# Performance work log

Measured on AMD Instinct MI355X. Metric: run time of the kernel, lower is better.

The kernel has to match this reference:

```python
import jax, jax.numpy as jnp
import numpy as np
import math

SCALES = [1, 2, 4, 8]
H = 1024           # hidden_size
NS = len(SCALES)
DS = H // NS       # per-scale dim = 256
NH_S = max(1, 8 // NS)  # heads per scale = 2


def _avg_pool(x, s):
    # x: [B, L, d], kernel=stride=s (L divisible by s)
    B, L, d = x.shape
    return x.reshape(B, L // s, s, d).mean(axis=2)


def _mha(q, k, v, in_w, in_b, out_w, out_b, nh):
    # torch nn.MultiheadAttention, batch_first, no mask.
    d = q.shape[-1]
    wq, wk, wv = in_w[:d], in_w[d:2 * d], in_w[2 * d:]
    bq, bk, bv = in_b[:d], in_b[d:2 * d], in_b[2 * d:]
    qh = q @ wq.T + bq
    kh = k @ wk.T + bk
    vh = v @ wv.T + bv
    B, Lq, _ = qh.shape
    Lk = kh.shape[1]
    hd = d // nh
    qh = qh.reshape(B, Lq, nh, hd).transpose(0, 2, 1, 3)
    kh = kh.reshape(B, Lk, nh, hd).transpose(0, 2, 1, 3)
    vh = vh.reshape(B, Lk, nh, hd).transpose(0, 2, 1, 3)
    scores = jnp.einsum('bhqd,bhkd->bhqk', qh, kh) * (1.0 / math.sqrt(hd))
    w = jax.nn.softmax(scores, axis=-1)
    out = jnp.einsum('bhqk,bhkd->bhqd', w, vh)
    out = out.transpose(0, 2, 1, 3).reshape(B, Lq, d)
    out = out @ out_w.T + out_b
    return out, w.mean(axis=1)  # averaged attn weights (torch default)


def setup_inputs() -> dict:
    key = jax.random.key(0)
    ks = jax.random.split(key, 20)
    B, S = 4, 2048
    f = lambda k, shape: (jax.random.normal(k, shape, dtype=jnp.float32) * 0.02)
    return {
        'query': jax.random.normal(ks[0], (B, S, H), dtype=jnp.float32),
        'key': jax.random.normal(ks[1], (B, S, H), dtype=jnp.float32),
        'value': jax.random.normal(ks[2], (B, S, H), dtype=jnp.float32),
        'wq': f(ks[3], (H, H)), 'bq': f(ks[4], (H,)),
        'wk': f(ks[5], (H, H)), 'bk': f(ks[6], (H,)),
        'wv': f(ks[7], (H, H)), 'bv': f(ks[8], (H,)),
        'mha_in_w': f(ks[9], (NS, 3 * DS, DS)),
        'mha_in_b': f(ks[10], (NS, 3 * DS)),
        'mha_out_w': f(ks[11], (NS, DS, DS)),
        'mha_out_b': f(ks[12], (NS, DS)),
        'fus_w': f(ks[13], (H, H)), 'fus_b': f(ks[14], (H,)),
    }


def reference(query, key, value, wq, bq, wk, bk, wv, bv,
              mha_in_w, mha_in_b, mha_out_w, mha_out_b, fus_w, fus_b):
    q = query @ wq.T + bq
    k = key @ wk.T + bk
    v = value @ wv.T + bv
    outs = []
    weights0 = None
    for i, s in enumerate(SCALES):
        qs = q[..., i * DS:(i + 1) * DS]
        ks_ = k[..., i * DS:(i + 1) * DS]
        vs = v[..., i * DS:(i + 1) * DS]
        if s > 1:
            ks_ = _avg_pool(ks_, s)
            vs = _avg_pool(vs, s)
        attended, w = _mha(qs, ks_, vs, mha_in_w[i], mha_in_b[i],
                           mha_out_w[i], mha_out_b[i], NH_S)
        # F.interpolate back to seq_len is an identity here (query length == seq_len)
        outs.append(attended)
        if i == 0:
            weights0 = w
    fused = jnp.concatenate(outs, axis=-1) @ fus_w.T + fus_b
    return fused, weights0
```

## Files before the change

### kernel.cpp

```cpp
#include <hip/hip_runtime.h>
#include <stdint.h>

typedef unsigned short u16;
typedef __bf16 v8bf __attribute__((ext_vector_type(8)));
typedef float v4f __attribute__((ext_vector_type(4)));
typedef __attribute__((address_space(3))) unsigned lds_t;
typedef const __attribute__((address_space(1))) unsigned g_t;

__device__ __forceinline__ u16 f2bf(float f) {
  union { float f; unsigned u; } v; v.f = f;
  unsigned r = v.u + 0x7FFFu + ((v.u >> 16) & 1u);
  return (u16)(r >> 16);
}
__device__ __forceinline__ float bf2f(u16 h) {
  union { unsigned u; float f; } v; v.u = ((unsigned)h) << 16;
  return v.f;
}
__device__ __forceinline__ ushort4 f4bf(float4 f) {
  ushort4 o;
  o.x = f2bf(f.x); o.y = f2bf(f.y); o.z = f2bf(f.z); o.w = f2bf(f.w);
  return o;
}

__global__ void k_cvt(const float* __restrict__ s, u16* __restrict__ d, long n) {
  long i = ((long)blockIdx.x * blockDim.x + threadIdx.x) * 4;
  long stride = (long)gridDim.x * blockDim.x * 4;
  for (; i < n; i += stride) {
    *(ushort4*)(d + i) = f4bf(*(const float4*)(s + i));
  }
}

__global__ void k_cvtpool(const float* __restrict__ src, u16* __restrict__ dst) {
  int g = blockIdx.x & 255, b = blockIdx.x >> 8;
  int c = threadIdx.x * 4;
  const float* p = src + ((long)b * 2048 + g * 8) * 1024 + c;
  u16* df = dst + ((long)b * 2048 + g * 8) * 1024 + c;
  float4 x[8];
#pragma unroll
  for (int j = 0; j < 8; j++) {
    x[j] = *(const float4*)(p + (long)j * 1024);
    *(ushort4*)(df + (long)j * 1024) = f4bf(x[j]);
  }
  float4 s2[4], s4[2], s8;
#pragma unroll
  for (int j = 0; j < 4; j++) {
    s2[j].x = x[2 * j].x + x[2 * j + 1].x;
    s2[j].y = x[2 * j].y + x[2 * j + 1].y;
    s2[j].z = x[2 * j].z + x[2 * j + 1].z;
    s2[j].w = x[2 * j].w + x[2 * j + 1].w;
  }
#pragma unroll
  for (int j = 0; j < 2; j++) {
    s4[j].x = s2[2 * j].x + s2[2 * j + 1].x;
    s4[j].y = s2[2 * j].y + s2[2 * j + 1].y;
    s4[j].z = s2[2 * j].z + s2[2 * j + 1].z;
    s4[j].w = s2[2 * j].w + s2[2 * j + 1].w;
  }
  s8.x = s4[0].x + s4[1].x; s8.y = s4[0].y + s4[1].y;
  s8.z = s4[0].z + s4[1].z; s8.w = s4[0].w + s4[1].w;
  u16* d2 = dst + ((long)8192 + b * 1024 + g * 4) * 1024 + c;
#pragma unroll
  for (int j = 0; j < 4; j++) {
    float4 t = {s2[j].x * 0.5f, s2[j].y * 0.5f, s2[j].z * 0.5f, s2[j].w * 0.5f};
    *(ushort4*)(d2 + (long)j * 1024) = f4bf(t);
  }
  u16* d4 = dst + ((long)12288 + b * 512 + g * 2) * 1024 + c;
#pragma unroll
  for (int j = 0; j < 2; j++) {
    float4 t = {s4[j].x * 0.25f, s4[j].y * 0.25f, s4[j].z * 0.25f, s4[j].w * 0.25f};
    *(ushort4*)(d4 + (long)j * 1024) = f4bf(t);
  }
  float4 t8 = {s8.x * 0.125f, s8.y * 0.125f, s8.z * 0.125f, s8.w * 0.125f};
  *(ushort4*)(dst + ((long)14336 + b * 256 + g) * 1024 + c) = f4bf(t8);
}

__global__ void k_tc(const float* __restrict__ src, u16* __restrict__ dst, int R, int C) {
  __shared__ float t[32][33];
  long zoff = (long)blockIdx.z * R * C;
  int r0 = blockIdx.y * 32, c0 = blockIdx.x * 32;
  int tx = threadIdx.x & 31, ty = threadIdx.x >> 5;
#pragma unroll
  for (int j = 0; j < 32; j += 8)
    t[ty + j][tx] = src[zoff + (long)(r0 + ty + j) * C + c0 + tx];
  __syncthreads();
#pragma unroll
  for (int j = 0; j < 32; j += 8)
    dst[zoff + (long)(c0 + ty + j) * R + r0 + tx] = f2bf(t[tx][ty + j]);
}

__global__ void k_bcomb_qkv(const float* __restrict__ in_w, const float* __restrict__ in_b,
                            const float* __restrict__ bq, const float* __restrict__ bk,
                            const float* __restrict__ bv, float* __restrict__ out) {
  int gw = (blockIdx.x * 256 + threadIdx.x) >> 6;
  int lane = threadIdx.x & 63;
  int p = gw >> 10, j = gw & 1023, i = j >> 8, of = j & 255;
  const float* bp = p == 0 ? bq : p == 1 ? bk : bv;
  const float* row = in_w + ((long)i * 768 + p * 256 + of) * 256;
  float s = 0.f;
#pragma unroll
  for (int m = 0; m < 4; m++) s += row[lane + m * 64] * bp[i * 256 + lane + m * 64];
#pragma unroll
  for (int m = 32; m >= 1; m >>= 1) s += __shfl_xor(s, m, 64);
  if (lane == 0) out[gw] = in_b[(long)i * 768 + p * 256 + of] + s;
}

__global__ void k_bcomb_f(const float* __restrict__ fw, const float* __restrict__ fb,
                          const float* __restrict__ ob, float* __restrict__ out) {
  int w = (blockIdx.x * 256 + threadIdx.x) >> 6;
  int lane = threadIdx.x & 63;
  const float* row = fw + (long)w * 1024;
  float s = 0.f;
  for (int k = lane; k < 1024; k += 64) s += row[k] * ob[k];
#pragma unroll
  for (int m = 32; m >= 1; m >>= 1) s += __shfl_xor(s, m, 64);
  if (lane == 0) out[w] = fb[w] + s;
}

__global__ __launch_bounds__(256) void k_ml0(
    const u16* __restrict__ QHf, const u16* __restrict__ KH,
    float* __restrict__ M0, float* __restrict__ L0)
{
  int z = blockIdx.z;
  int b = z >> 1, h = z & 1;
  int q0 = blockIdx.y * 64;
  __shared__ u16 KV[2][128][32];
  __shared__ float red[2][4][64];

  const int tid = threadIdx.x, lane = tid & 63, wave = tid >> 6;
  const int q4 = lane >> 4, l16 = lane & 15;
  const int wr = (wave >> 1) * 32, wc = (wave & 1) * 64;
  const int srow = wave * 16 + (lane >> 2), scol = (lane & 3) * 8;
  const float alpha = 0.08838834764831845f;

  v8bf qf[2][4];
#pragma unroll
  for (int mi = 0; mi < 2; mi++)
#pragma unroll
    for (int sub = 0; sub < 4; sub++)
      qf[mi][sub] = *(const v8bf*)(QHf + ((long)b * 2048 + q0 + wr + mi * 16 + l16) * 1024
                                   + h * 128 + sub * 32 + q4 * 8);

  const u16* gK = KH + (long)b * 2048 * 256 + h * 128;
  auto stageK = [&](int buf, int kt, int sub) {
    const u16* g = gK + (long)(kt * 128 + srow) * 256 + sub * 32 + scol;
    __builtin_amdgcn_global_load_lds((g_t*)g, (lds_t*)&KV[buf][wave * 16][0], 16, 0, 0);
    __builtin_amdgcn_global_load_lds((g_t*)(g + 64 * 256), (lds_t*)&KV[buf][64 + wave * 16][0], 16, 0, 0);
  };

  float m_run[2][4], l_run[2][4];
#pragma unroll
  for (int mi = 0; mi < 2; mi++)
#pragma unroll
    for (int i4 = 0; i4 < 4; i4++) { m_run[mi][i4] = -1e30f; l_run[mi][i4] = 0.f; }

  for (int kt = 0; kt < 16; kt++) {
    v4f s[2][4];
#pragma unroll
    for (int mi = 0; mi < 2; mi++)
#pragma unroll
      for (int ni = 0; ni < 4; ni++) s[mi][ni] = (v4f){0.f, 0.f, 0.f, 0.f};
    stageK(0, kt, 0);
    __syncthreads();
    int cur = 0;
#pragma unroll
    for (int sub = 0; sub < 4; sub++) {
      if (sub < 3) stageK(cur ^ 1, kt, sub + 1);
      v8bf kf[4];
#pragma unroll
      for (int ni = 0; ni < 4; ni++)
        kf[ni] = *(const v8bf*)&KV[cur][wc + ni * 16 + l16][q4 * 8];
#pragma unroll
      for (int mi = 0; mi < 2; mi++)
#pragma unroll
        for (int ni = 0; ni < 4; ni++)
          s[mi][ni] = __builtin_amdgcn_mfma_f32_16x16x32_bf16(qf[mi][sub], kf[ni], s[mi][ni], 0, 0, 0);
      __syncthreads();
      cur ^= 1;
    }
#pragma unroll
    for (int mi = 0; mi < 2; mi++)
#pragma unroll
      for (int ni = 0; ni < 4; ni++) s[mi][ni] *= alpha;
    float mloc[2][4];
#pragma unroll
    for (int mi = 0; mi < 2; mi++)
#pragma unroll
      for (int i4 = 0; i4 < 4; i4++)
        mloc[mi][i4] = fmaxf(fmaxf(s[mi][0][i4], s[mi][1][i4]),
                             fmaxf(s[mi][2][i4], s[mi][3][i4]));
#pragma unroll
    for (int d = 1; d <= 8; d <<= 1)
#pragma unroll
      for (int mi = 0; mi < 2; mi++)
#pragma unroll
        for (int i4 = 0; i4 < 4; i4++)
          mloc[mi][i4] = fmaxf(mloc[mi][i4], __shfl_xor(mloc[mi][i4], d, 64));
    if (l16 == 0) {
#pragma unroll
      for (int mi = 0; mi < 2; mi++)
#pragma unroll
        for (int i4 = 0; i4 < 4; i4++)
          red[0][wave][wr + mi * 16 + q4 * 4 + i4] = mloc[mi][i4];
    }
    __syncthreads();
    float lloc[2][4] = {{0.f, 0.f, 0.f, 0.f}, {0.f, 0.f, 0.f, 0.f}};
#pragma unroll
    for (int mi = 0; mi < 2; mi++)
#pragma unroll
      for (int i4 = 0; i4 < 4; i4++) {
        int rr = wr + mi * 16 + q4 * 4 + i4;
        float mn = fmaxf(fmaxf(red[0][wave][rr], red[0][wave ^ 1][rr]), m_run[mi][i4]);
        float scl = __expf(m_run[mi][i4] - mn);
        m_run[mi][i4] = mn;
        l_run[mi][i4] *= scl;
#pragma unroll
        for (int ni = 0; ni < 4; ni++)
          lloc[mi][i4] += __expf(s[mi][ni][i4] - mn);
      }
#pragma unroll
    for (int d = 1; d <= 8; d <<= 1)
#pragma unroll
      for (int mi = 0; mi < 2; mi++)
#pragma unroll
        for (int i4 = 0; i4 < 4; i4++)
          lloc[mi][i4] += __shfl_xor(lloc[mi][i4], d, 64);
    if (l16 == 0) {
#pragma unroll
      for (int mi = 0; mi < 2; mi++)
#pragma unroll
        for (int i4 = 0; i4 < 4; i4++)
          red[1][wave][wr + mi * 16 + q4 * 4 + i4] = lloc[mi][i4];
    }
    __syncthreads();
#pragma unroll
    for (int mi = 0; mi < 2; mi++)
#pragma unroll
      for (int i4 = 0; i4 < 4; i4++) {
        int rr = wr + mi * 16 + q4 * 4 + i4;
        l_run[mi][i4] += red[1][wave][rr] + red[1][wave ^ 1][rr];
      }
    __syncthreads();
  }

  if ((wave & 1) == 0 && l16 == 0) {
#pragma unroll
    for (int mi = 0; mi < 2; mi++)
#pragma unroll
      for (int i4 = 0; i4 < 4; i4++) {
        int r = q0 + wr + mi * 16 + q4 * 4 + i4;
        M0[(long)z * 2048 + r] = m_run[mi][i4];
        L0[(long)z * 2048 + r] = l_run[mi][i4];
      }
  }
}

__global__ __launch_bounds__(256) void k_pv0(
    const u16* __restrict__ QHf, const u16* __restrict__ KH,
    const u16* __restrict__ VHT, const float* __restrict__ M0,
    const float* __restrict__ L0, u16* __restrict__ AOf, float* __restrict__ W0)
{
  int b = blockIdx.z;
  int q0 = blockIdx.y * 32;
  __shared__ u16 P[2][32][136];
  __shared__ u16 KV[2][128][32];

  const int tid = threadIdx.x, lane = tid & 63, wave = tid >> 6;
  const int q4 = lane >> 4, l16 = lane & 15;
  const int wr = (wave >> 1) * 16, wc = (wave & 1) * 64;
  const int srow = wave * 16 + (lane >> 2), scol = (lane & 3) * 8;
  const float alpha = 0.08838834764831845f;

  v8bf qf[2][4];
#pragma unroll
  for (int h = 0; h < 2; h++)
#pragma unroll
    for (int sub = 0; sub < 4; sub++)
      qf[h][sub] = *(const v8bf*)(QHf + ((long)b * 2048 + q0 + wr + l16) * 1024
                                  + h * 128 + sub * 32 + q4 * 8);
  float mv[2][4], il[2][4];
#pragma unroll
  for (int h = 0; h < 2; h++)
#pragma unroll
    for (int i4 = 0; i4 < 4; i4++) {
      long r = (long)(b * 2 + h) * 2048 + q0 + wr + q4 * 4 + i4;
      mv[h][i4] = M0[r];
      il[h][i4] = 1.0f / L0[r];
    }

  const u16* gK = KH + (long)b * 2048 * 256;
  auto stageK = [&](int buf, int h, int kt, int sub) {
    const u16* g = gK + (long)(kt * 128 + srow) * 256 + h * 128 + sub * 32 + scol;
    __builtin_amdgcn_global_load_lds((g_t*)g, (lds_t*)&KV[buf][wave * 16][0], 16, 0, 0);
    __builtin_amdgcn_global_load_lds((g_t*)(g + 64 * 256), (lds_t*)&KV[buf][64 + wave * 16][0], 16, 0, 0);
  };
  auto stageV = [&](int buf, int h, int kt, int sub) {
    const u16* g = VHT + ((long)(b * 2 + h) * 128 + srow) * 2048 + kt * 128 + sub * 32 + scol;
    __builtin_amdgcn_global_load_lds((g_t*)g, (lds_t*)&KV[buf][wave * 16][0], 16, 0, 0);
    __builtin_amdgcn_global_load_lds((g_t*)(g + (long)64 * 2048), (lds_t*)&KV[buf][64 + wave * 16][0], 16, 0, 0);
  };

  v4f acc[2][4];
#pragma unroll
  for (int h = 0; h < 2; h++)
#pragma unroll
    for (int ni = 0; ni < 4; ni++) acc[h][ni] = (v4f){0.f, 0.f, 0.f, 0.f};

  for (int kt = 0; kt < 16; kt++) {
    float p0[4][4];
#pragma unroll
    for (int h = 0; h < 2; h++) {
      v4f s[4];
#pragma unroll
      for (int ni = 0; ni < 4; ni++) s[ni] = (v4f){0.f, 0.f, 0.f, 0.f};
      stageK(0, h, kt, 0);
      __syncthreads();
      int cur = 0;
#pragma unroll
      for (int sub = 0; sub < 4; sub++) {
        if (sub < 3) stageK(cur ^ 1, h, kt, sub + 1);
        v8bf kf[4];
#pragma unroll
        for (int ni = 0; ni < 4; ni++)
          kf[ni] = *(const v8bf*)&KV[cur][wc + ni * 16 + l16][q4 * 8];
#pragma unroll
        for (int ni = 0; ni < 4; ni++)
          s[ni] = __builtin_amdgcn_mfma_f32_16x16x32_bf16(qf[h][sub], kf[ni], s[ni], 0, 0, 0);
        __syncthreads();
        cur ^= 1;
      }
#pragma unroll
      for (int ni = 0; ni < 4; ni++)
#pragma unroll
        for (int i4 = 0; i4 < 4; i4++) {
          float p = __expf(s[ni][i4] * alpha - mv[h][i4]) * il[h][i4];
          P[h][wr + q4 * 4 + i4][wc + ni * 16 + l16] = f2bf(p);
          if (h == 0) p0[ni][i4] = p;
          else {
            W0[((long)b * 2048 + q0 + wr + q4 * 4 + i4) * 2048
               + kt * 128 + wc + ni * 16 + l16] = 0.5f * (p0[ni][i4] + p);
          }
        }
    }
#pragma unroll
    for (int h = 0; h < 2; h++) {
      stageV(0, h, kt, 0);
      __syncthreads();
      int cv = 0;
#pragma unroll
      for (int sub = 0; sub < 4; sub++) {
        if (sub < 3) stageV(cv ^ 1, h, kt, sub + 1);
        v8bf pf = *(const v8bf*)&P[h][wr + l16][sub * 32 + q4 * 8];
        v8bf vf[4];
#pragma unroll
        for (int ni = 0; ni < 4; ni++)
          vf[ni] = *(const v8bf*)&KV[cv][wc + ni * 16 + l16][q4 * 8];
#pragma unroll
        for (int ni = 0; ni < 4; ni++)
          acc[h][ni] = __builtin_amdgcn_mfma_f32_16x16x32_bf16(pf, vf[ni], acc[h][ni], 0, 0, 0);
        __syncthreads();
        cv ^= 1;
      }
    }
  }

#pragma unroll
  for (int h = 0; h < 2; h++)
#pragma unroll
    for (int ni = 0; ni < 4; ni++)
#pragma unroll
      for (int i4 = 0; i4 < 4; i4++) {
        int r = q0 + wr + q4 * 4 + i4;
        int c = wc + ni * 16 + l16;
        AOf[((long)b * 2048 + r) * 1024 + h * 128 + c] = f2bf(acc[h][ni][i4]);
      }
}

__global__ __launch_bounds__(256) void k_flash(
    const u16* __restrict__ QHf, const u16* __restrict__ KH,
    const u16* __restrict__ VHT, u16* __restrict__ AOf)
{
  int z = blockIdx.z;
  int i = (z >> 3) + 1;
  int b = (z >> 1) & 3, h = z & 1;
  int Ls = 2048 >> i;
  int nkt = Ls >> 7;
  long ro = (long)(16384 - (8192 >> (i - 1))) * 256;
  int q0 = blockIdx.y * 64;

  __shared__ u16 QP[64][136];
  __shared__ u16 KV[2][128][32];
  __shared__ float red[2][4][64];

  const int tid = threadIdx.x, lane = tid & 63, wave = tid >> 6;
  const int q4 = lane >> 4, l16 = lane & 15;
  const int wr = (wave >> 1) * 32, wc = (wave & 1) * 64;
  const int srow = wave * 16 + (lane >> 2);
  const int scol = (lane & 3) * 8;

  {
    const u16* gq = QHf + ((long)b * 2048 + q0) * 1024 + i * 256 + h * 128;
    int idx = tid * 4;
#pragma unroll
    for (int j = 0; j < 4; j++) {
      int r = (idx + j) >> 4, ch = (idx + j) & 15;
      *(ulonglong2*)&QP[r][ch * 8] = *(const ulonglong2*)(gq + (long)r * 1024 + ch * 8);
    }
  }
  __syncthreads();
  v8bf qf[2][4];
#pragma unroll
  for (int mi = 0; mi < 2; mi++)
#pragma unroll
    for (int sub = 0; sub < 4; sub++)
      qf[mi][sub] = *(const v8bf*)&QP[wr + mi * 16 + l16][sub * 32 + q4 * 8];
  __syncthreads();

  const u16* gK = KH + ro + (long)b * Ls * 256 + h * 128;
  const u16* gV = VHT + ro + (long)(b * 2 + h) * 128 * Ls;

  auto stageK = [&](int buf, int kt, int sub) {
    const u16* g = gK + (long)(kt * 128 + srow) * 256 + sub * 32 + scol;
    __builtin_amdgcn_global_load_lds((g_t*)g, (lds_t*)&KV[buf][wave * 16][0], 16, 0, 0);
    __builtin_amdgcn_global_load_lds((g_t*)(g + 64 * 256), (lds_t*)&KV[buf][64 + wave * 16][0], 16, 0, 0);
  };
  auto stageV = [&](int buf, int kt, int sub) {
    const u16* g = gV + (long)srow * Ls + kt * 128 + sub * 32 + scol;
    __builtin_amdgcn_global_load_lds((g_t*)g, (lds_t*)&KV[buf][wave * 16][0], 16, 0, 0);
    __builtin_amdgcn_global_load_lds((g_t*)(g + (long)64 * Ls), (lds_t*)&KV[buf][64 + wave * 16][0], 16, 0, 0);
  };

  v4f acc_o[2][4];
  float m_run[2][4], l_run[2][4];
#pragma unroll
  for (int mi = 0; mi < 2; mi++)
#pragma unroll
    for (int ni = 0; ni < 4; ni++) acc_o[mi][ni] = (v4f){0.f, 0.f, 0.f, 0.f};
#pragma unroll
  for (int mi = 0; mi < 2; mi++)
#pragma unroll
    for (int i4 = 0; i4 < 4; i4++) { m_run[mi][i4] = -1e30f; l_run[mi][i4] = 0.f; }

  const float alpha = 0.08838834764831845f;

  for (int kt = 0; kt < nkt; kt++) {
    v4f s[2][4];
#pragma unroll
    for (int mi = 0; mi < 2; mi++)
#pragma unroll
      for (int ni = 0; ni < 4; ni++) s[mi][ni] = (v4f){0.f, 0.f, 0.f, 0.f};
    stageK(0, kt, 0);
    __syncthreads();
    int cur = 0;
#pragma unroll
    for (int sub = 0; sub < 4; sub++) {
      if (sub < 3) stageK(cur ^ 1, kt, sub + 1);
      v8bf kf[4];
#pragma unroll
      for (int ni = 0; ni < 4; ni++)
        kf[ni] = *(const v8bf*)&KV[cur][wc + ni * 16 + l16][q4 * 8];
#pragma unroll
      for (int mi = 0; mi < 2; mi++)
#pragma unroll
        for (int ni = 0; ni < 4; ni++)
          s[mi][ni] = __builtin_amdgcn_mfma_f32_16x16x32_bf16(qf[mi][sub], kf[ni], s[mi][ni], 0, 0, 0);
      __syncthreads();
      cur ^= 1;
    }
    stageV(0, kt, 0);

#pragma unroll
    for (int mi = 0; mi < 2; mi++)
#pragma unroll
      for (int ni = 0; ni < 4; ni++) s[mi][ni] *= alpha;
    float mloc[2][4];
#pragma unroll
    for (int mi = 0; mi < 2; mi++)
#pragma unroll
      for (int i4 = 0; i4 < 4; i4++)
        mloc[mi][i4] = fmaxf(fmaxf(s[mi][0][i4], s[mi][1][i4]),
                             fmaxf(s[mi][2][i4], s[mi][3][i4]));
#pragma unroll
    for (int d = 1; d <= 8; d <<= 1)
#pragma unroll
      for (int mi = 0; mi < 2; mi++)
#pragma unroll
        for (int i4 = 0; i4 < 4; i4++)
          mloc[mi][i4] = fmaxf(mloc[mi][i4], __shfl_xor(mloc[mi][i4], d, 64));
    if (l16 == 0) {
#pragma unroll
      for (int mi = 0; mi < 2; mi++)
#pragma unroll
        for (int i4 = 0; i4 < 4; i4++)
          red[0][wave][wr + mi * 16 + q4 * 4 + i4] = mloc[mi][i4];
    }
    __syncthreads();
    float scl[2][4];
#pragma unroll
    for (int mi = 0; mi < 2; mi++)
#pragma unroll
      for (int i4 = 0; i4 < 4; i4++) {
        int rr = wr + mi * 16 + q4 * 4 + i4;
        float mn = fmaxf(fmaxf(red[0][wave][rr], red[0][wave ^ 1][rr]), m_run[mi][i4]);
        scl[mi][i4] = __expf(m_run[mi][i4] - mn);
        m_run[mi][i4] = mn;
      }
    float lloc[2][4] = {{0.f, 0.f, 0.f, 0.f}, {0.f, 0.f, 0.f, 0.f}};
#pragma unroll
    for (int mi = 0; mi < 2; mi++)
#pragma unroll
      for (int ni = 0; ni < 4; ni++)
#pragma unroll
        for (int i4 = 0; i4 < 4; i4++) {
          float p = __expf(s[mi][ni][i4] - m_run[mi][i4]);
          lloc[mi][i4] += p;
          QP[wr + mi * 16 + q4 * 4 + i4][wc + ni * 16 + l16] = f2bf(p);
        }
#pragma unroll
    for (int d = 1; d <= 8; d <<= 1)
#pragma unroll
      for (int mi = 0; mi < 2; mi++)
#pragma unroll
        for (int i4 = 0; i4 < 4; i4++)
          lloc[mi][i4] += __shfl_xor(lloc[mi][i4], d, 64);
    if (l16 == 0) {
#pragma unroll
      for (int mi = 0; mi < 2; mi++)
#pragma unroll
        for (int i4 = 0; i4 < 4; i4++)
          red[1][wave][wr + mi * 16 + q4 * 4 + i4] = lloc[mi][i4];
    }
#pragma unroll
    for (int mi = 0; mi < 2; mi++)
#pragma unroll
      for (int ni = 0; ni < 4; ni++)
#pragma unroll
        for (int i4 = 0; i4 < 4; i4++) acc_o[mi][ni][i4] *= scl[mi][i4];
    __syncthreads();
#pragma unroll
    for (int mi = 0; mi < 2; mi++)
#pragma unroll
      for (int i4 = 0; i4 < 4; i4++) {
        int rr = wr + mi * 16 + q4 * 4 + i4;
        l_run[mi][i4] = l_run[mi][i4] * scl[mi][i4] + red[1][wave][rr] + red[1][wave ^ 1][rr];
      }

    int cv = 0;
#pragma unroll
    for (int sub = 0; sub < 4; sub++) {
      if (sub < 3) stageV(cv ^ 1, kt, sub + 1);
      v8bf pf[2], vf[4];
#pragma unroll
      for (int mi = 0; mi < 2; mi++)
        pf[mi] = *(const v8bf*)&QP[wr + mi * 16 + l16][sub * 32 + q4 * 8];
#pragma unroll
      for (int ni = 0; ni < 4; ni++)
        vf[ni] = *(const v8bf*)&KV[cv][wc + ni * 16 + l16][q4 * 8];
#pragma unroll
      for (int mi = 0; mi < 2; mi++)
#pragma unroll
        for (int ni = 0; ni < 4; ni++)
          acc_o[mi][ni] = __builtin_amdgcn_mfma_f32_16x16x32_bf16(pf[mi], vf[ni], acc_o[mi][ni], 0, 0, 0);
      __syncthreads();
      cv ^= 1;
    }
  }

#pragma unroll
  for (int mi = 0; mi < 2; mi++)
#pragma unroll
    for (int i4 = 0; i4 < 4; i4++) {
      float inv = 1.0f / l_run[mi][i4];
#pragma unroll
      for (int ni = 0; ni < 4; ni++) {
        int r = q0 + wr + mi * 16 + q4 * 4 + i4;
        int c = wc + ni * 16 + l16;
        AOf[((long)b * 2048 + r) * 1024 + i * 256 + h * 128 + c] =
            f2bf(acc_o[mi][ni][i4] * inv);
      }
    }
}

template<int WBF>
__global__ __launch_bounds__(256) void k_gemm(
    const u16* __restrict__ A, long ldA, long sA1, long sA2,
    const u16* __restrict__ B, long ldB, long sB1, long sB2,
    void* __restrict__ Cv, long ldC, long sC1, long sC2, long sCk,
    const float* __restrict__ bias, long sBias, float alpha,
    int M, int N, int K, int nz2, int KS)
{
  __shared__ u16 As[2][128][32];
  __shared__ u16 Bs[2][128][32];
  int z = blockIdx.z;
  int ks = z % KS; int zz = z / KS;
  int z1 = zz / nz2, z2 = zz - z1 * nz2;
  A += (long)z1 * sA1 + (long)z2 * sA2 + (long)ks * K;
  B += (long)z1 * sB1 + (long)z2 * sB2 + (long)ks * K;
  long coff = (long)z1 * sC1 + (long)z2 * sC2 + (long)ks * sCk;
  const float* bz = bias ? bias + (long)z2 * sBias : nullptr;
  const int m0 = blockIdx.y * 128, n0 = blockIdx.x * 128;
  const int tid = threadIdx.x;
  const int lane = tid & 63;
  const int wave = tid >> 6;
  const int wr = (wave >> 1) * 64, wc = (wave & 1) * 64;
  const int q4 = lane >> 4, l16 = lane & 15;

  const int srow = wave * 16 + (lane >> 2);
  const int scol = (lane & 3) * 8;
  const u16* gA = A + (long)(m0 + srow) * ldA + scol;
  const u16* gB = B + (long)(n0 + srow) * ldB + scol;

  auto stage = [&](int buf, int kt) {
    __builtin_amdgcn_global_load_lds((g_t*)(gA + kt), (lds_t*)&As[buf][wave * 16][0], 16, 0, 0);
    __builtin_amdgcn_global_load_lds((g_t*)(gA + 64 * ldA + kt), (lds_t*)&As[buf][64 + wave * 16][0], 16, 0, 0);
    __builtin_amdgcn_global_load_lds((g_t*)(gB + kt), (lds_t*)&Bs[buf][wave * 16][0], 16, 0, 0);
    __builtin_amdgcn_global_load_lds((g_t*)(gB + 64 * ldB + kt), (lds_t*)&Bs[buf][64 + wave * 16][0], 16, 0, 0);
  };

  v4f acc[4][4];
#pragma unroll
  for (int i = 0; i < 4; i++)
#pragma unroll
    for (int j = 0; j < 4; j++) acc[i][j] = (v4f){0.f, 0.f, 0.f, 0.f};

  stage(0, 0);
  __syncthreads();
  int cur = 0;
  for (int kt = 0; kt < K; kt += 32) {
    if (kt + 32 < K) stage(cur ^ 1, kt + 32);
    v8bf af[4], bf[4];
#pragma unroll
    for (int i = 0; i < 4; i++) af[i] = *(const v8bf*)&As[cur][wr + i * 16 + l16][q4 * 8];
#pragma unroll
    for (int i = 0; i < 4; i++) bf[i] = *(const v8bf*)&Bs[cur][wc + i * 16 + l16][q4 * 8];
#pragma unroll
    for (int mi = 0; mi < 4; mi++)
#pragma unroll
      for (int ni = 0; ni < 4; ni++)
        acc[mi][ni] = __builtin_amdgcn_mfma_f32_16x16x32_bf16(af[mi], bf[ni], acc[mi][ni], 0, 0, 0);
    __syncthreads();
    cur ^= 1;
  }

#pragma unroll
  for (int mi = 0; mi < 4; mi++) {
    int rb = m0 + wr + mi * 16 + q4 * 4;
#pragma unroll
    for (int ni = 0; ni < 4; ni++) {
      int c = n0 + wc + ni * 16 + l16;
      float bv = bz ? bz[c] : 0.f;
#pragma unroll
      for (int i = 0; i < 4; i++) {
        int r = rb + i;
        float val = acc[mi][ni][i] * alpha + bv;
        if (WBF) ((u16*)Cv)[coff + (long)r * ldC + c] = f2bf(val);
        else     ((float*)Cv)[coff + (long)r * ldC + c] = val;
      }
    }
  }
}

__global__ __launch_bounds__(256) void k_gemm_kv(
    const u16* __restrict__ Xk, const u16* __restrict__ Xv,
    const u16* __restrict__ WCkv, const float* __restrict__ Bckv,
    u16* __restrict__ KH, u16* __restrict__ VHT)
{
  __shared__ u16 As[2][128][32];
  __shared__ u16 Bs[2][128][32];
  const int isV = blockIdx.z;
  const int m0 = blockIdx.y * 128, n0 = blockIdx.x * 128;
  const int scale = m0 < 8192 ? 0 : (m0 < 12288 ? 1 : (m0 < 14336 ? 2 : 3));
  const int rbase = scale == 0 ? 0 : (scale == 1 ? 8192 : (scale == 2 ? 12288 : 14336));
  const int lsh = 11 - scale;
  const u16* A = isV ? Xv : Xk;
  const u16* B = WCkv + (long)isV * 1048576 + (long)scale * 262144;
  const float* bz = Bckv + isV * 1024 + scale * 256;

  const int tid = threadIdx.x;
  const int lane = tid & 63, wave = tid >> 6;
  const int wr = (wave >> 1) * 64, wc = (wave & 1) * 64;
  const int q4 = lane >> 4, l16 = lane & 15;
  const int srow = wave * 16 + (lane >> 2);
  const int scol = (lane & 3) * 8;
  const u16* gA = A + (long)(m0 + srow) * 1024 + scol;
  const u16* gB = B + (long)(n0 + srow) * 1024 + scol;

  auto stage = [&](int buf, int kt) {
    __builtin_amdgcn_global_load_lds((g_t*)(gA + kt), (lds_t*)&As[buf][wave * 16][0], 16, 0, 0);
    __builtin_amdgcn_global_load_lds((g_t*)(gA + 64 * 1024 + kt), (lds_t*)&As[buf][64 + wave * 16][0], 16, 0, 0);
    __builtin_amdgcn_global_load_lds((g_t*)(gB + kt), (lds_t*)&Bs[buf][wave * 16][0], 16, 0, 0);
    __builtin_amdgcn_global_load_lds((g_t*)(gB + 64 * 1024 + kt), (lds_t*)&Bs[buf][64 + wave * 16][0], 16, 0, 0);
  };

  v4f acc[4][4];
#pragma unroll
  for (int i = 0; i < 4; i++)
#pragma unroll
    for (int j = 0; j < 4; j++) acc[i][j] = (v4f){0.f, 0.f, 0.f, 0.f};

  stage(0, 0);
  __syncthreads();
  int cur = 0;
  for (int kt = 0; kt < 1024; kt += 32) {
    if (kt + 32 < 1024) stage(cur ^ 1, kt + 32);
    v8bf af[4], bf[4];
#pragma unroll
    for (int i = 0; i < 4; i++) af[i] = *(const v8bf*)&As[cur][wr + i * 16 + l16][q4 * 8];
#pragma unroll
    for (int i = 0; i < 4; i++) bf[i] = *(const v8bf*)&Bs[cur][wc + i * 16 + l16][q4 * 8];
#pragma unroll
    for (int mi = 0; mi < 4; mi++)
#pragma unroll
      for (int ni = 0; ni < 4; ni++)
        acc[mi][ni] = __builtin_amdgcn_mfma_f32_16x16x32_bf16(af[mi], bf[ni], acc[mi][ni], 0, 0, 0);
    __syncthreads();
    cur ^= 1;
  }

#pragma unroll
  for (int mi = 0; mi < 4; mi++) {
    int rb = m0 + wr + mi * 16 + q4 * 4;
#pragma unroll
    for (int ni = 0; ni < 4; ni++) {
      int c = n0 + wc + ni * 16 + l16;
      float bv = bz[c];
#pragma unroll
      for (int i = 0; i < 4; i++) {
        int r = rb + i;
        float val = acc[mi][ni][i] + bv;
        if (!isV) {
          KH[(long)r * 256 + c] = f2bf(val);
        } else {
          int rl = r - rbase;
          int b = rl >> lsh, t = rl & ((1 << lsh) - 1);
          int h = c >> 7, n = c & 127;
          VHT[(long)rbase * 256 + (((long)(b * 2 + h) * 128 + n) << lsh) + t] = f2bf(val);
        }
      }
    }
  }
}

extern "C" void kernel_launch(void* const* d_in, const int* in_sizes, int n_in,
                              void* d_out, int out_size, void* d_ws, size_t ws_size,
                              hipStream_t stream) {
  const float* query = (const float*)d_in[0];
  const float* key_  = (const float*)d_in[1];
  const float* value = (const float*)d_in[2];
  const float* wq    = (const float*)d_in[3];
  const float* bq    = (const float*)d_in[4];
  const float* wk    = (const float*)d_in[5];
  const float* bk    = (const float*)d_in[6];
  const float* wv    = (const float*)d_in[7];
  const float* bv    = (const float*)d_in[8];
  const float* in_w  = (const float*)d_in[9];
  const float* in_b  = (const float*)d_in[10];
  const float* out_w = (const float*)d_in[11];
  const float* out_b = (const float*)d_in[12];
  const float* fus_w = (const float*)d_in[13];
  const float* fus_b = (const float*)d_in[14];
  (void)in_sizes; (void)n_in; (void)out_size; (void)ws_size;

  float* outF  = (float*)d_out;
  float* outW0 = outF + (long)4 * 2048 * 1024;

  char* base = (char*)d_ws;
  size_t off = 0;
  auto alloc = [&](size_t bytes) -> void* {
    void* p = base + off;
    off = (off + bytes + 255) & ~(size_t)255;
    return p;
  };
  const long NX = (long)8192 * 1024;
  u16* Winb = (u16*)alloc((size_t)4 * 768 * 256 * 2);
  u16* Wfb  = (u16*)alloc((size_t)1024 * 1024 * 2);
  u16* WoT  = (u16*)alloc((size_t)4 * 256 * 256 * 2);
  u16* WT   = (u16*)alloc((size_t)3 * 1024 * 1024 * 2);
  u16* WC   = (u16*)alloc((size_t)3 * 1024 * 1024 * 2);
  u16* WFc  = (u16*)alloc((size_t)1024 * 1024 * 2);
  float* Bc  = (float*)alloc((size_t)3 * 1024 * 4);
  float* fbc = (float*)alloc((size_t)1024 * 4);
  u16* Xq    = (u16*)alloc((size_t)NX * 2);
  u16* XkAll = (u16*)alloc((size_t)15360 * 1024 * 2);
  u16* XvAll = (u16*)alloc((size_t)15360 * 1024 * 2);
  u16* QHf = (u16*)alloc((size_t)8192 * 1024 * 2);
  u16* KH  = (u16*)alloc((size_t)15360 * 256 * 2);
  u16* VHT = (u16*)alloc((size_t)15360 * 256 * 2);
  float* M0 = (float*)alloc((size_t)8 * 2048 * 4);
  float* L0 = (float*)alloc((size_t)8 * 2048 * 4);
  u16* AOf = (u16*)alloc((size_t)8192 * 1024 * 2);

  k_cvt<<<1024, 256, 0, stream>>>(query, Xq, NX);
  k_cvtpool<<<1024, 256, 0, stream>>>(key_,  XkAll);
  k_cvtpool<<<1024, 256, 0, stream>>>(value, XvAll);
  k_cvt<<<192, 256, 0, stream>>>(in_w, Winb, 4 * 768 * 256);
  k_cvt<<<256, 256, 0, stream>>>(fus_w, Wfb, 1024 * 1024);
  k_tc<<<dim3(32, 32, 1), 256, 0, stream>>>(wq, WT, 1024, 1024);
  k_tc<<<dim3(32, 32, 1), 256, 0, stream>>>(wk, WT + (long)1024 * 1024, 1024, 1024);
  k_tc<<<dim3(32, 32, 1), 256, 0, stream>>>(wv, WT + (long)2 * 1024 * 1024, 1024, 1024);
  k_tc<<<dim3(8, 8, 4), 256, 0, stream>>>(out_w, WoT, 256, 256);
  k_bcomb_qkv<<<768, 256, 0, stream>>>(in_w, in_b, bq, bk, bv, Bc);
  k_bcomb_f<<<256, 256, 0, stream>>>(fus_w, fus_b, out_b, fbc);

  k_gemm<1><<<dim3(8, 2, 12), 256, 0, stream>>>(
      Winb, 256, 65536, 196608,
      WT, 1024, 1048576, 256,
      WC, 1024, 1048576, 262144, 0,
      nullptr, 0, 1.f, 256, 1024, 256, 4, 1);
  k_gemm<1><<<dim3(2, 8, 4), 256, 0, stream>>>(
      Wfb, 1024, 0, 256,
      WoT, 256, 0, 65536,
      WFc, 1024, 0, 256, 0,
      nullptr, 0, 1.f, 1024, 256, 256, 4, 1);

  k_gemm<1><<<dim3(8, 64, 1), 256, 0, stream>>>(
      Xq, 1024, 0, 0, WC, 1024, 0, 0,
      QHf, 1024, 0, 0, 0, Bc, 0, 1.f, 8192, 1024, 1024, 1, 1);
  k_gemm_kv<<<dim3(2, 120, 2), 256, 0, stream>>>(
      XkAll, XvAll, WC + (long)1024 * 1024, Bc + 1024, KH, VHT);

  k_ml0<<<dim3(1, 32, 8), 256, 0, stream>>>(QHf, KH, M0, L0);
  k_pv0<<<dim3(1, 64, 4), 256, 0, stream>>>(QHf, KH, VHT, M0, L0, AOf, outW0);

  k_flash<<<dim3(1, 32, 24), 256, 0, stream>>>(QHf, KH, VHT, AOf);

  k_gemm<0><<<dim3(8, 64, 1), 256, 0, stream>>>(
      AOf, 1024, 0, 0, WFc, 1024, 0, 0,
      outF, 1024, 0, 0, 0, fbc, 0, 1.f, 8192, 1024, 1024, 1, 1);
}
```

Baseline: 552.2 us.

## Split scale-0 attention key range across blocks with partial reductions

Splits the key dimension of the scale-0 row-stats and PV kernels into four chunks launched as separate blocks, so each launch has four times as many blocks. Partial max/sum values are merged in a new combine kernel. Partial PV outputs are written as fp32 and summed into the bf16 output by a separate reduction kernel. This targets low occupancy (256 blocks) on a many-CU GPU, at the cost of extra fp32 traffic (about 32 MB of partials) and two more launches.

```diff
diff --git a/kernel.cpp b/kernel.cpp
--- a/kernel.cpp
+++ b/kernel.cpp
@@ -116,10 +116,25 @@
   if (lane == 0) out[w] = fb[w] + s;
 }
 
+template<int KS>
+__global__ __launch_bounds__(256) void k_ksum(const float* __restrict__ P,
+                                              u16* __restrict__ O, long n, int coloff) {
+  long i = ((long)blockIdx.x * 256 + threadIdx.x) * 4;
+  if (i >= n) return;
+  float4 s = *(const float4*)(P + i);
+#pragma unroll
+  for (int ks = 1; ks < KS; ks++) {
+    float4 t = *(const float4*)(P + (long)ks * n + i);
+    s.x += t.x; s.y += t.y; s.z += t.z; s.w += t.w;
+  }
+  *(ushort4*)(O + (i >> 8) * 1024 + coloff + (int)(i & 255)) = f4bf(s);
+}
+
 __global__ __launch_bounds__(256) void k_ml0(
     const u16* __restrict__ QHf, const u16* __restrict__ KH,
-    float* __restrict__ M0, float* __restrict__ L0)
+    float* __restrict__ Mp, float* __restrict__ Lp)
 {
+  int kc = blockIdx.x;
   int z = blockIdx.z;
   int b = z >> 1, h = z & 1;
   int q0 = blockIdx.y * 64;
@@ -153,7 +168,7 @@
 #pragma unroll
     for (int i4 = 0; i4 < 4; i4++) { m_run[mi][i4] = -1e30f; l_run[mi][i4] = 0.f; }
 
-  for (int kt = 0; kt < 16; kt++) {
+  for (int kt = kc * 4; kt < kc * 4 + 4; kt++) {
     v4f s[2][4];
 #pragma unroll
     for (int mi = 0; mi < 2; mi++)
@@ -243,22 +258,39 @@
   }
 
   if ((wave & 1) == 0 && l16 == 0) {
+    long zo = ((long)kc * 8 + z) * 2048;
 #pragma unroll
     for (int mi = 0; mi < 2; mi++)
 #pragma unroll
       for (int i4 = 0; i4 < 4; i4++) {
         int r = q0 + wr + mi * 16 + q4 * 4 + i4;
-        M0[(long)z * 2048 + r] = m_run[mi][i4];
-        L0[(long)z * 2048 + r] = l_run[mi][i4];
-      }
-  }
+        Mp[zo + r] = m_run[mi][i4];
+        Lp[zo + r] = l_run[mi][i4];
+      }
+  }
+}
+
+__global__ __launch_bounds__(256) void k_mlcomb(
+    const float* __restrict__ Mp, const float* __restrict__ Lp,
+    float* __restrict__ M0, float* __restrict__ L0)
+{
+  long r = (long)blockIdx.x * 256 + threadIdx.x;
+  float m = -1e30f;
+#pragma unroll
+  for (int kc = 0; kc < 4; kc++) m = fmaxf(m, Mp[kc * 16384 + r]);
+  float l = 0.f;
+#pragma unroll
+  for (int kc = 0; kc < 4; kc++)
+    l += Lp[kc * 16384 + r] * __expf(Mp[kc * 16384 + r] - m);
+  M0[r] = m; L0[r] = l;
 }
 
 __global__ __launch_bounds__(256) void k_pv0(
     const u16* __restrict__ QHf, const u16* __restrict__ KH,
     const u16* __restrict__ VHT, const float* __restrict__ M0,
-    const float* __restrict__ L0, u16* __restrict__ AOf, float* __restrict__ W0)
+    const float* __restrict__ L0, float* __restrict__ PP, float* __restrict__ W0)
 {
+  int kc = blockIdx.x;
   int b = blockIdx.z;
   int q0 = blockIdx.y * 32;
   __shared__ u16 P[2][32][136];
@@ -305,7 +337,7 @@
 #pragma unroll
     for (int ni = 0; ni < 4; ni++) acc[h][ni] = (v4f){0.f, 0.f, 0.f, 0.f};
 
-  for (int kt = 0; kt < 16; kt++) {
+  for (int kt = kc * 4; kt < kc * 4 + 4; kt++) {
     float p0[4][4];
 #pragma unroll
     for (int h = 0; h < 2; h++) {
@@ -363,6 +395,7 @@
     }
   }
 
+  float* pp = PP + ((long)kc * 8192 + (long)b * 2048) * 256;
 #pragma unroll
   for (int h = 0; h < 2; h++)
 #pragma unroll
@@ -371,7 +404,7 @@
       for (int i4 = 0; i4 < 4; i4++) {
         int r = q0 + wr + q4 * 4 + i4;
         int c = wc + ni * 16 + l16;
-        AOf[((long)b * 2048 + r) * 1024 + h * 128 + c] = f2bf(acc[h][ni][i4]);
+        pp[(long)r * 256 + h * 128 + c] = acc[h][ni][i4];
       }
 }
 
@@ -787,7 +820,12 @@
   u16* VHT = (u16*)alloc((size_t)15360 * 256 * 2);
   float* M0 = (float*)alloc((size_t)8 * 2048 * 4);
   float* L0 = (float*)alloc((size_t)8 * 2048 * 4);
+  float* Mp = (float*)alloc((size_t)4 * 8 * 2048 * 4);
+  float* Lp = (float*)alloc((size_t)4 * 8 * 2048 * 4);
+  float* PP = (float*)alloc((size_t)4 * 8192 * 256 * 4);
   u16* AOf = (u16*)alloc((size_t)8192 * 1024 * 2);
+
+  const long AOsz = (long)8192 * 256;
 
   k_cvt<<<1024, 256, 0, stream>>>(query, Xq, NX);
   k_cvtpool<<<1024, 256, 0, stream>>>(key_,  XkAll);
@@ -818,8 +856,10 @@
   k_gemm_kv<<<dim3(2, 120, 2), 256, 0, stream>>>(
       XkAll, XvAll, WC + (long)1024 * 1024, Bc + 1024, KH, VHT);
 
-  k_ml0<<<dim3(1, 32, 8), 256, 0, stream>>>(QHf, KH, M0, L0);
-  k_pv0<<<dim3(1, 64, 4), 256, 0, stream>>>(QHf, KH, VHT, M0, L0, AOf, outW0);
+  k_ml0<<<dim3(4, 32, 8), 256, 0, stream>>>(QHf, KH, Mp, Lp);
+  k_mlcomb<<<64, 256, 0, stream>>>(Mp, Lp, M0, L0);
+  k_pv0<<<dim3(4, 64, 4), 256, 0, stream>>>(QHf, KH, VHT, M0, L0, PP, outW0);
+  k_ksum<4><<<2048, 256, 0, stream>>>(PP, AOf, AOsz, 0);
 
   k_flash<<<dim3(1, 32, 24), 256, 0, stream>>>(QHf, KH, VHT, AOf);
 
```

After: 518.8 us. 1.06x faster.
